# Performance work log

Hardware: AMD Instinct MI355X
Metric: run time of the kernel (lower is better)

Reference implementation:

```python
import jax, jax.numpy as jnp
import numpy as np

B, S, A, H, N = 4096, 128, 32, 1024, 256
BETA = 1.0            # params['temperature']
NORM_SMOOTHING = 0.01 # params['norm_smoothing']
MAX_A = 1.0           # env.action_space.high[0]
# dropout_rate = 0.0 and eval-mode reference -> dropout is identity


def setup_inputs() -> dict:
    key = jax.random.key(0)
    ks = jax.random.split(key, 16)
    sc_s = 1.0 / np.sqrt(S)
    sc_h = 1.0 / np.sqrt(H)
    return {
        "s": jax.random.normal(ks[0], (B, S), jnp.float32),
        "a": jax.random.normal(ks[1], (B, A), jnp.float32),
        # value side MLP: S->H->H->H->N
        "Wv1": jax.random.uniform(ks[2], (S, H), jnp.float32, -sc_s, sc_s),
        "bv1": jax.random.uniform(ks[3], (H,), jnp.float32, -sc_s, sc_s),
        "Wv2": jax.random.uniform(ks[4], (H, H), jnp.float32, -sc_h, sc_h),
        "bv2": jax.random.uniform(ks[5], (H,), jnp.float32, -sc_h, sc_h),
        "Wv3": jax.random.uniform(ks[6], (H, H), jnp.float32, -sc_h, sc_h),
        "bv3": jax.random.uniform(ks[7], (H,), jnp.float32, -sc_h, sc_h),
        "Wv4": jax.random.uniform(ks[8], (H, N), jnp.float32, -sc_h, sc_h),
        "bv4": jax.random.uniform(ks[9], (N,), jnp.float32, -sc_h, sc_h),
        # location side: S->H (xavier), then N expert linears H->A stacked
        "Wl1": jax.random.normal(ks[10], (S, H), jnp.float32) * np.sqrt(2.0 / (S + H)),
        "bl1": jnp.zeros((H,), jnp.float32),
        "Wexp": jax.random.uniform(ks[11], (N, H, A), jnp.float32, -0.1, 0.1),
        "bexp": jax.random.uniform(ks[12], (N, A), jnp.float32, -1.0, 1.0),
    }


def reference(s, a, Wv1, bv1, Wv2, bv2, Wv3, bv3, Wv4, bv4, Wl1, bl1, Wexp, bexp):
    t = jax.nn.relu(s @ Wv1 + bv1)
    t = jax.nn.relu(t @ Wv2 + bv2)
    t = jax.nn.relu(t @ Wv3 + bv3)
    values = t @ Wv4 + bv4                      # [B, N]

    # --- get_all_centroids: shared hidden, N expert heads as grouped GEMM ---
    h = jax.nn.relu(s @ Wl1 + bl1)              # [B, H] (dropout identity)
    centroids = MAX_A * jnp.tanh(
        jnp.einsum("bh,nha->bna", h, Wexp) + bexp[None]
    )                                           # [B, N, A]

    # --- rbf_function: softmax over -beta * ||centroid - a|| ---
    diff = centroids - a[:, None, :]            # [B, N, A]
    dist = jnp.sqrt(jnp.sum(diff * diff, axis=2) + NORM_SMOOTHING)  # [B, N]
    weights = jax.nn.softmax(-BETA * dist, axis=1)                  # [B, N]

    return jnp.sum(weights * values, axis=1, keepdims=True)         # [B, 1]
```

## Files before the change

kernel.cpp:

```cpp
#include <hip/hip_runtime.h>
#include <hip/hip_bf16.h>


typedef _Float16 half8 __attribute__((ext_vector_type(8)));
typedef _Float16 half4v __attribute__((ext_vector_type(4)));
typedef float floatx16 __attribute__((ext_vector_type(16)));

namespace {
constexpr int kB = 4096, kS = 128, kA = 32, kH = 1024, kN = 256;
constexpr size_t al(size_t x) { return (x + 255) & ~size_t(255); }
constexpr size_t OFF_FLAG  = 0;
constexpr size_t OFF_S16   = 256;
constexpr size_t OFF_WEXPT = OFF_S16   + al((size_t)kB * kS * 2);
constexpr size_t OFF_BUF2  = OFF_WEXPT + al((size_t)kN * kA * kH * 2);
constexpr size_t OFF_VAL   = OFF_BUF2  + al((size_t)kB * kH * 2);
constexpr size_t OFF_WV1T  = OFF_VAL   + al((size_t)kB * kN * 4);
constexpr size_t OFF_WV2T  = OFF_WV1T  + al((size_t)kS * kH * 2);
constexpr size_t OFF_WV3T  = OFF_WV2T  + al((size_t)kH * kH * 2);
constexpr size_t OFF_WV4T  = OFF_WV3T  + al((size_t)kH * kH * 2);
constexpr size_t OFF_WL1T  = OFF_WV4T  + al((size_t)kH * kN * 2);
constexpr size_t OFF_BUF1  = OFF_WL1T  + al((size_t)kS * kH * 2);
constexpr size_t OFF_Z     = OFF_WV1T;
}

__device__ __forceinline__ float ldraw(const void* p, size_t i, int bf) {
    if (bf) return __uint_as_float(((unsigned)((const unsigned short*)p)[i]) << 16);
    return ((const float*)p)[i];
}

__device__ __forceinline__ float4 ldraw4(const void* p, size_t i, int bf) {
    if (bf) {
        ushort4 u = *(const ushort4*)((const unsigned short*)p + i);
        return make_float4(__uint_as_float((unsigned)u.x << 16),
                           __uint_as_float((unsigned)u.y << 16),
                           __uint_as_float((unsigned)u.z << 16),
                           __uint_as_float((unsigned)u.w << 16));
    }
    return *(const float4*)((const float*)p + i);
}

__device__ __forceinline__ void gl_lds16(const _Float16* g, _Float16* l) {
    __builtin_amdgcn_global_load_lds(
        (const __attribute__((address_space(1))) unsigned int*)g,
        (__attribute__((address_space(3))) unsigned int*)l, 16, 0, 0);
}

__device__ __forceinline__ float fast_tanh(float x) {
    x = fminf(9.f, fmaxf(-9.f, x));
    float e = __expf(2.f * x);
    return (e - 1.f) * __builtin_amdgcn_rcpf(e + 1.f);
}

__global__ void detect_kernel(const unsigned int* __restrict__ s_raw, int* __restrict__ flag) {
    __shared__ int cnt;
    if (threadIdx.x == 0) cnt = 0;
    __syncthreads();
    const unsigned e = (s_raw[threadIdx.x] >> 7) & 0xFFu;
    int c = (e >= 118u && e <= 135u) ? 1 : 0;
    for (int off = 32; off > 0; off >>= 1) c += __shfl_down(c, off);
    if ((threadIdx.x & 63) == 0) atomicAdd(&cnt, c);
    __syncthreads();
    if (threadIdx.x == 0) *flag = (cnt > 128) ? 1 : 0;
}

__global__ void convert_to_f16(const void* __restrict__ src, _Float16* __restrict__ dst,
                               int n, const int* __restrict__ flag) {
    const int bf = *flag;
    int i = blockIdx.x * blockDim.x + threadIdx.x;
    const int stride = gridDim.x * blockDim.x;
    for (; i < n; i += stride) dst[i] = (_Float16)ldraw(src, i, bf);
}

struct TDesc { const void* src; _Float16* dst; int K; int N; int tiles; };
struct TPack { TDesc d[6]; };

__global__ void transpose_all(TPack p, const int* __restrict__ flag) {
    __shared__ float tile[32][33];
    const int bf = *flag;
    int bid = blockIdx.x;
    int i = 0;
    while (bid >= p.d[i].tiles) { bid -= p.d[i].tiles; ++i; }
    const int K = p.d[i].K, N = p.d[i].N;
    const int tpz = (N >> 5) * (K >> 5);
    const int z = bid / tpz, r = bid - z * tpz;
    const int n0 = (r % (N >> 5)) * 32, k0 = (r / (N >> 5)) * 32;
    const size_t zo = (size_t)z * K * N;
    const void* src = p.d[i].src;
    _Float16* dst = p.d[i].dst;
    const int tx = threadIdx.x, ty = threadIdx.y;
    float4 v = ldraw4(src, zo + (size_t)(k0 + ty) * N + n0 + tx * 4, bf);
    tile[ty][tx * 4 + 0] = v.x;
    tile[ty][tx * 4 + 1] = v.y;
    tile[ty][tx * 4 + 2] = v.z;
    tile[ty][tx * 4 + 3] = v.w;
    __syncthreads();
    half4v o;
#pragma unroll
    for (int j = 0; j < 4; ++j) o[j] = (_Float16)tile[tx * 4 + j][ty];
    *(half4v*)(dst + zo + (size_t)(n0 + ty) * K + k0 + tx * 4) = o;
}

template <int TM, int TN, int DO_RELU, int OUT_F16>
__launch_bounds__(256, (TM == 128 ? 2 : 4))
__global__ void dgemm(const _Float16* __restrict__ A, const _Float16* __restrict__ Bt,
                      const void* __restrict__ bias_raw, void* __restrict__ Cout,
                      const int* __restrict__ flagp, int N, int K) {
    constexpr int BK = 32;
    constexpr int MI = TM / 64, NI = TN / 64;
    constexpr int ACH = TM * BK / 8;
    constexpr int BCH = TN * BK / 8;
    constexpr int AT = ACH / 256, BT = BCH / 256;
    __shared__ _Float16 As[2 * ACH * 8];
    __shared__ _Float16 Bs[2 * BCH * 8];

    const int tid = threadIdx.x;
    const int lane = tid & 63;
    const int w = tid >> 6, wr = w >> 1, wc = w & 1;
    const int m0 = blockIdx.x * TM, n0 = blockIdx.y * TN;

    const _Float16* gAsrc[AT];
    _Float16* lAdst[AT];
#pragma unroll
    for (int t = 0; t < AT; ++t) {
        const int c = t * 256 + tid;
        const int ks = c / (TM * 2), rem = c % (TM * 2);
        const int row = (rem >> 6) * 32 + (rem & 31);
        const int kcol = ks * 16 + ((rem >> 5) & 1) * 8;
        gAsrc[t] = A + (size_t)(m0 + row) * K + kcol;
        lAdst[t] = As + c * 8;
    }
    const _Float16* gBsrc[BT];
    _Float16* lBdst[BT];
#pragma unroll
    for (int t = 0; t < BT; ++t) {
        const int c = t * 256 + tid;
        const int ks = c / (TN * 2), rem = c % (TN * 2);
        const int row = (rem >> 6) * 32 + (rem & 31);
        const int kcol = ks * 16 + ((rem >> 5) & 1) * 8;
        gBsrc[t] = Bt + (size_t)(n0 + row) * K + kcol;
        lBdst[t] = Bs + c * 8;
    }

    auto issue = [&](int k0, int st) {
#pragma unroll
        for (int t = 0; t < AT; ++t) gl_lds16(gAsrc[t] + k0, lAdst[t] + st * ACH * 8);
#pragma unroll
        for (int t = 0; t < BT; ++t) gl_lds16(gBsrc[t] + k0, lBdst[t] + st * BCH * 8);
    };

    floatx16 acc[MI][NI];
#pragma unroll
    for (int mi = 0; mi < MI; ++mi)
#pragma unroll
        for (int ni = 0; ni < NI; ++ni)
#pragma unroll
            for (int i = 0; i < 16; ++i) acc[mi][ni][i] = 0.f;

    auto compute = [&](int st) {
#pragma unroll
        for (int ks = 0; ks < 2; ++ks) {
            half8 af[MI], bf[NI];
#pragma unroll
            for (int mi = 0; mi < MI; ++mi)
                af[mi] = *(const half8*)(As + st * ACH * 8 + ((size_t)(ks * TM * 2 + (wr * MI + mi) * 64 + lane)) * 8);
#pragma unroll
            for (int ni = 0; ni < NI; ++ni)
                bf[ni] = *(const half8*)(Bs + st * BCH * 8 + ((size_t)(ks * TN * 2 + (wc * NI + ni) * 64 + lane)) * 8);
#pragma unroll
            for (int mi = 0; mi < MI; ++mi)
#pragma unroll
                for (int ni = 0; ni < NI; ++ni)
                    acc[mi][ni] = __builtin_amdgcn_mfma_f32_32x32x16_f16(af[mi], bf[ni], acc[mi][ni], 0, 0, 0);
        }
    };

    issue(0, 0);
    for (int k0 = 0; k0 < K; k0 += 2 * BK) {
        __syncthreads();
        if (k0 + BK < K) issue(k0 + BK, 1);
        compute(0);
        __syncthreads();
        if (k0 + 2 * BK < K) issue(k0 + 2 * BK, 0);
        compute(1);
    }

    const int bf_ = *flagp;
    const int am = lane & 31;
    const int half = lane >> 5;
#pragma unroll
    for (int mi = 0; mi < MI; ++mi)
#pragma unroll
        for (int ni = 0; ni < NI; ++ni) {
            const int Rb = m0 + (wr * MI + mi) * 32;
            const int Cb = n0 + (wc * NI + ni) * 32 + am;
            const float bv = ldraw(bias_raw, Cb, bf_);
#pragma unroll
            for (int rr = 0; rr < 16; ++rr) {
                const int row = Rb + (rr & 3) + 8 * (rr >> 2) + 4 * half;
                float x = acc[mi][ni][rr] + bv;
                if (DO_RELU) x = fmaxf(x, 0.f);
                if (OUT_F16) ((_Float16*)Cout)[(size_t)row * N + Cb] = (_Float16)x;
                else ((float*)Cout)[(size_t)row * N + Cb] = x;
            }
        }
}

__launch_bounds__(256)
__global__ void final_fused(const _Float16* __restrict__ z, const void* __restrict__ a_raw,
                            const float* __restrict__ values, const int* __restrict__ flag,
                            void* __restrict__ out) {
    const int b = blockIdx.x;
    const int n = threadIdx.x;
    const int bf = *flag;
    __shared__ float as_[32];
    if (n < 32) as_[n] = ldraw(a_raw, (size_t)b * kA + n, bf);
    __syncthreads();

    const _Float16* zp = z + (size_t)b * (kN * kA) + n * kA;
    float zl[32];
#pragma unroll
    for (int t = 0; t < 4; ++t) {
        half8 h = *(const half8*)(zp + t * 8);
#pragma unroll
        for (int j = 0; j < 8; ++j) zl[t * 8 + j] = (float)h[j];
    }
    float sum = 0.f;
#pragma unroll
    for (int a = 0; a < 32; ++a) {
        const float c = fast_tanh(zl[a]);
        const float d = c - as_[a];
        sum = fmaf(d, d, sum);
    }
    const float dist = sqrtf(sum + 0.01f);
    const float v = values[(size_t)b * kN + n];

    const int wid = n >> 6, lane = n & 63;
    __shared__ float red[8];
    __shared__ float rw[4], rwv[4];
    float m = dist;
    for (int off = 32; off > 0; off >>= 1) m = fminf(m, __shfl_down(m, off));
    if (lane == 0) red[wid] = m;
    __syncthreads();
    if (n == 0) red[4] = fminf(fminf(red[0], red[1]), fminf(red[2], red[3]));
    __syncthreads();
    const float dmin = red[4];

    float wgt = expf(dmin - dist);
    float wv = wgt * v;
    for (int off = 32; off > 0; off >>= 1) {
        wgt += __shfl_down(wgt, off);
        wv += __shfl_down(wv, off);
    }
    if (lane == 0) { rw[wid] = wgt; rwv[wid] = wv; }
    __syncthreads();
    if (n == 0) {
        const float sw = rw[0] + rw[1] + rw[2] + rw[3];
        const float swv = rwv[0] + rwv[1] + rwv[2] + rwv[3];
        const float o = swv / sw;
        if (bf) ((__hip_bfloat16*)out)[b] = __float2bfloat16(o);
        else    ((float*)out)[b] = o;
    }
}

extern "C" void kernel_launch(void* const* d_in, const int* in_sizes, int n_in,
                              void* d_out, int out_size, void* d_ws, size_t ws_size,
                              hipStream_t stream) {
    (void)in_sizes; (void)n_in; (void)out_size; (void)ws_size;
    char* ws = (char*)d_ws;
    int* flag = (int*)(ws + OFF_FLAG);
    _Float16* s16   = (_Float16*)(ws + OFF_S16);
    _Float16* wv1t  = (_Float16*)(ws + OFF_WV1T);
    _Float16* wv2t  = (_Float16*)(ws + OFF_WV2T);
    _Float16* wv3t  = (_Float16*)(ws + OFF_WV3T);
    _Float16* wv4t  = (_Float16*)(ws + OFF_WV4T);
    _Float16* wl1t  = (_Float16*)(ws + OFF_WL1T);
    _Float16* wexpt = (_Float16*)(ws + OFF_WEXPT);
    _Float16* buf1  = (_Float16*)(ws + OFF_BUF1);
    _Float16* buf2  = (_Float16*)(ws + OFF_BUF2);
    float* values   = (float*)(ws + OFF_VAL);
    _Float16* z     = (_Float16*)(ws + OFF_Z);

    detect_kernel<<<1, 256, 0, stream>>>((const unsigned int*)d_in[0], flag);
    convert_to_f16<<<512, 256, 0, stream>>>(d_in[0], s16, kB * kS, flag);

    TPack tp;
    tp.d[0] = {d_in[2],  wv1t,  kS, kH, (kH / 32) * (kS / 32)};
    tp.d[1] = {d_in[4],  wv2t,  kH, kH, (kH / 32) * (kH / 32)};
    tp.d[2] = {d_in[6],  wv3t,  kH, kH, (kH / 32) * (kH / 32)};
    tp.d[3] = {d_in[8],  wv4t,  kH, kN, (kN / 32) * (kH / 32)};
    tp.d[4] = {d_in[10], wl1t,  kS, kH, (kH / 32) * (kS / 32)};
    tp.d[5] = {d_in[12], wexpt, kH, kA, kN * (kA / 32) * (kH / 32)};
    int total_tiles = 0;
    for (int i = 0; i < 6; ++i) total_tiles += tp.d[i].tiles;
    transpose_all<<<total_tiles, dim3(8, 32), 0, stream>>>(tp, flag);

    dgemm<64, 64, 1, 1><<<dim3(kB / 64, kH / 64), 256, 0, stream>>>(s16,  wv1t, d_in[3], buf1, flag, kH, kS);
    dgemm<128, 64, 1, 1><<<dim3(kB / 128, kH / 64), 256, 0, stream>>>(buf1, wv2t, d_in[5], buf2, flag, kH, kH);
    dgemm<128, 64, 1, 1><<<dim3(kB / 128, kH / 64), 256, 0, stream>>>(buf2, wv3t, d_in[7], buf1, flag, kH, kH);
    dgemm<64, 64, 0, 0><<<dim3(kB / 64, kN / 64), 256, 0, stream>>>(buf1, wv4t, d_in[9], values, flag, kN, kH);
    dgemm<64, 64, 1, 1><<<dim3(kB / 64, kH / 64), 256, 0, stream>>>(s16,  wl1t, d_in[11], buf2, flag, kH, kS);
    dgemm<128, 128, 0, 1><<<dim3(kB / 128, (kN * kA) / 128), 256, 0, stream>>>(buf2, wexpt, d_in[13], z, flag, kN * kA, kH);
    final_fused<<<kB, 256, 0, stream>>>(z, d_in[1], values, flag, d_out);
}
```

Before: 342.9 us.

## Switch dgemm to 16x16x32 MFMA with BK=64 single-buffered LDS

Rewrites the dense GEMM to use 16x16x32 f16 MFMA tiles instead of 32x32x16, doubles the K-step to 64, and replaces the double-buffered LDS pipeline with a single buffer that is loaded, synchronized and then consumed. It also drops the occupancy hint from the launch bounds. The intent is fewer loop iterations and barriers per K and a different register and occupancy balance. In exchange, global-to-LDS loads no longer overlap with MFMA compute, and the smaller MFMA shape does less reuse per fragment load.

```diff
diff --git a/kernel.cpp b/kernel.cpp
--- a/kernel.cpp
+++ b/kernel.cpp
@@ -4,7 +4,7 @@
 
 typedef _Float16 half8 __attribute__((ext_vector_type(8)));
 typedef _Float16 half4v __attribute__((ext_vector_type(4)));
-typedef float floatx16 __attribute__((ext_vector_type(16)));
+typedef float floatx4 __attribute__((ext_vector_type(4)));
 
 namespace {
 constexpr int kB = 4096, kS = 128, kA = 32, kH = 1024, kN = 256;
@@ -101,106 +101,93 @@
 }
 
 template <int TM, int TN, int DO_RELU, int OUT_F16>
-__launch_bounds__(256, (TM == 128 ? 2 : 4))
+__launch_bounds__(256)
 __global__ void dgemm(const _Float16* __restrict__ A, const _Float16* __restrict__ Bt,
                       const void* __restrict__ bias_raw, void* __restrict__ Cout,
                       const int* __restrict__ flagp, int N, int K) {
-    constexpr int BK = 32;
-    constexpr int MI = TM / 64, NI = TN / 64;
+    constexpr int BK = 64;
+    constexpr int MI = TM / 32, NI = TN / 32;
     constexpr int ACH = TM * BK / 8;
     constexpr int BCH = TN * BK / 8;
     constexpr int AT = ACH / 256, BT = BCH / 256;
-    __shared__ _Float16 As[2 * ACH * 8];
-    __shared__ _Float16 Bs[2 * BCH * 8];
+    __shared__ _Float16 As[ACH * 8];
+    __shared__ _Float16 Bs[BCH * 8];
 
     const int tid = threadIdx.x;
     const int lane = tid & 63;
-    const int w = tid >> 6, wr = w >> 1, wc = w & 1;
+    const int wr = (tid >> 6) >> 1, wc = (tid >> 6) & 1;
     const int m0 = blockIdx.x * TM, n0 = blockIdx.y * TN;
+    const int lrow = lane & 15, lkc = lane >> 4;
 
     const _Float16* gAsrc[AT];
     _Float16* lAdst[AT];
 #pragma unroll
     for (int t = 0; t < AT; ++t) {
         const int c = t * 256 + tid;
-        const int ks = c / (TM * 2), rem = c % (TM * 2);
-        const int row = (rem >> 6) * 32 + (rem & 31);
-        const int kcol = ks * 16 + ((rem >> 5) & 1) * 8;
+        const int kb = c / (TM * 4), rem = c % (TM * 4);
+        const int row = (rem >> 6) * 16 + lrow;
+        const int kcol = kb * 32 + lkc * 8;
         gAsrc[t] = A + (size_t)(m0 + row) * K + kcol;
-        lAdst[t] = As + c * 8;
+        lAdst[t] = As + (size_t)c * 8;
     }
     const _Float16* gBsrc[BT];
     _Float16* lBdst[BT];
 #pragma unroll
     for (int t = 0; t < BT; ++t) {
         const int c = t * 256 + tid;
-        const int ks = c / (TN * 2), rem = c % (TN * 2);
-        const int row = (rem >> 6) * 32 + (rem & 31);
-        const int kcol = ks * 16 + ((rem >> 5) & 1) * 8;
+        const int kb = c / (TN * 4), rem = c % (TN * 4);
+        const int row = (rem >> 6) * 16 + lrow;
+        const int kcol = kb * 32 + lkc * 8;
         gBsrc[t] = Bt + (size_t)(n0 + row) * K + kcol;
-        lBdst[t] = Bs + c * 8;
-    }
-
-    auto issue = [&](int k0, int st) {
-#pragma unroll
-        for (int t = 0; t < AT; ++t) gl_lds16(gAsrc[t] + k0, lAdst[t] + st * ACH * 8);
-#pragma unroll
-        for (int t = 0; t < BT; ++t) gl_lds16(gBsrc[t] + k0, lBdst[t] + st * BCH * 8);
-    };
-
-    floatx16 acc[MI][NI];
+        lBdst[t] = Bs + (size_t)c * 8;
+    }
+
+    floatx4 acc[MI][NI];
 #pragma unroll
     for (int mi = 0; mi < MI; ++mi)
 #pragma unroll
         for (int ni = 0; ni < NI; ++ni)
 #pragma unroll
-            for (int i = 0; i < 16; ++i) acc[mi][ni][i] = 0.f;
-
-    auto compute = [&](int st) {
-#pragma unroll
-        for (int ks = 0; ks < 2; ++ks) {
-            half8 af[MI], bf[NI];
+            for (int i = 0; i < 4; ++i) acc[mi][ni][i] = 0.f;
+
+    for (int k0 = 0; k0 < K; k0 += BK) {
+#pragma unroll
+        for (int t = 0; t < AT; ++t) gl_lds16(gAsrc[t] + k0, lAdst[t]);
+#pragma unroll
+        for (int t = 0; t < BT; ++t) gl_lds16(gBsrc[t] + k0, lBdst[t]);
+        __syncthreads();
+#pragma unroll
+        for (int kb = 0; kb < 2; ++kb) {
+            half8 af[MI], bfr[NI];
 #pragma unroll
             for (int mi = 0; mi < MI; ++mi)
-                af[mi] = *(const half8*)(As + st * ACH * 8 + ((size_t)(ks * TM * 2 + (wr * MI + mi) * 64 + lane)) * 8);
+                af[mi] = *(const half8*)(As + ((size_t)((kb * (TM / 16) + wr * MI + mi) * 64 + lane)) * 8);
 #pragma unroll
             for (int ni = 0; ni < NI; ++ni)
-                bf[ni] = *(const half8*)(Bs + st * BCH * 8 + ((size_t)(ks * TN * 2 + (wc * NI + ni) * 64 + lane)) * 8);
+                bfr[ni] = *(const half8*)(Bs + ((size_t)((kb * (TN / 16) + wc * NI + ni) * 64 + lane)) * 8);
 #pragma unroll
             for (int mi = 0; mi < MI; ++mi)
 #pragma unroll
                 for (int ni = 0; ni < NI; ++ni)
-                    acc[mi][ni] = __builtin_amdgcn_mfma_f32_32x32x16_f16(af[mi], bf[ni], acc[mi][ni], 0, 0, 0);
+                    acc[mi][ni] = __builtin_amdgcn_mfma_f32_16x16x32_f16(af[mi], bfr[ni], acc[mi][ni], 0, 0, 0);
         }
-    };
-
-    issue(0, 0);
-    for (int k0 = 0; k0 < K; k0 += 2 * BK) {
         __syncthreads();
-        if (k0 + BK < K) issue(k0 + BK, 1);
-        compute(0);
-        __syncthreads();
-        if (k0 + 2 * BK < K) issue(k0 + 2 * BK, 0);
-        compute(1);
     }
 
     const int bf_ = *flagp;
-    const int am = lane & 31;
-    const int half = lane >> 5;
 #pragma unroll
     for (int mi = 0; mi < MI; ++mi)
 #pragma unroll
         for (int ni = 0; ni < NI; ++ni) {
-            const int Rb = m0 + (wr * MI + mi) * 32;
-            const int Cb = n0 + (wc * NI + ni) * 32 + am;
+            const int Rb = m0 + (wr * MI + mi) * 16 + lkc * 4;
+            const int Cb = n0 + (wc * NI + ni) * 16 + lrow;
             const float bv = ldraw(bias_raw, Cb, bf_);
 #pragma unroll
-            for (int rr = 0; rr < 16; ++rr) {
-                const int row = Rb + (rr & 3) + 8 * (rr >> 2) + 4 * half;
-                float x = acc[mi][ni][rr] + bv;
+            for (int r = 0; r < 4; ++r) {
+                float x = acc[mi][ni][r] + bv;
                 if (DO_RELU) x = fmaxf(x, 0.f);
-                if (OUT_F16) ((_Float16*)Cout)[(size_t)row * N + Cb] = (_Float16)x;
-                else ((float*)Cout)[(size_t)row * N + Cb] = x;
+                if (OUT_F16) ((_Float16*)Cout)[(size_t)(Rb + r) * N + Cb] = (_Float16)x;
+                else ((float*)Cout)[(size_t)(Rb + r) * N + Cb] = x;
             }
         }
 }
```

Result: no change. 348.7 us (+1.7%).
